# Optimization experiments

Hardware: AMD Instinct MI355X
Metric: run time of the kernel (lower is better)

The kernel has to match this reference:

```python
import jax, jax.numpy as jnp
import numpy as np
from jax import lax

TEMP = 0.1  # softmax_temp default in forward


def _conv(x, w, b):
    y = lax.conv_general_dilated(x, w, (1, 1), 'VALID',
                                 dimension_numbers=('NCHW', 'OIHW', 'NCHW'))
    return y + b[None, :, None, None]


def _avg_pool2(x):
    # AvgPool2d(2,2), floor mode (VALID window)
    s = lax.reduce_window(x, 0.0, lax.add, (1, 1, 2, 2), (1, 1, 2, 2), 'VALID')
    return s / 4.0


def _cnn(x, c1w, c1b, c2w, c2b, c3w, c3b, dw, db):
    x = _avg_pool2(jax.nn.relu(_conv(x, c1w, c1b)))   # (N,8,13,13)
    x = _avg_pool2(jax.nn.relu(_conv(x, c2w, c2b)))   # (N,16,5,5)
    x = _avg_pool2(jax.nn.relu(_conv(x, c3w, c3b)))   # (N,32,1,1)
    x = x.reshape(x.shape[0], -1)                      # (N,32)
    logits = x @ dw.T + db                             # (N,10)
    return jax.nn.softmax(logits, axis=1)


def _digit_to_rule(p):
    # p: (N,10) -> (N,6)
    return jnp.stack([p[:, 8], p[:, 4] + p[:, 6], p[:, 0] + p[:, 2],
                      p[:, 7] + p[:, 9], p[:, 5], p[:, 1] + p[:, 3]], axis=1)


def setup_inputs() -> dict:
    key = jax.random.key(0)
    ks = jax.random.split(key, 10)
    B, T, D, C, H, W = 256, 8, 4, 1, 28, 28
    sc = 0.1
    return {
        'sequences': jax.random.normal(ks[0], (B, T, D, C, H, W), jnp.float32),
        'conv1_w': jax.random.normal(ks[1], (8, 1, 3, 3), jnp.float32) * sc,
        'conv1_b': jax.random.normal(ks[2], (8,), jnp.float32) * sc,
        'conv2_w': jax.random.normal(ks[3], (16, 8, 3, 3), jnp.float32) * sc,
        'conv2_b': jax.random.normal(ks[4], (16,), jnp.float32) * sc,
        'conv3_w': jax.random.normal(ks[5], (32, 16, 3, 3), jnp.float32) * sc,
        'conv3_b': jax.random.normal(ks[6], (32,), jnp.float32) * sc,
        'dense_w': jax.random.normal(ks[7], (10, 32), jnp.float32) * sc,
        'dense_b': jax.random.normal(ks[8], (10,), jnp.float32) * sc,
        'trans': jax.nn.softmax(jax.random.normal(ks[9], (6, 9, 10), jnp.float32), axis=-1),
    }


def reference(sequences, conv1_w, conv1_b, conv2_w, conv2_b, conv3_w, conv3_b,
              dense_w, dense_b, trans):
    B, T, D, C, H, W = sequences.shape
    S = trans.shape[2]           # num_states = 10
    N = T * D                    # number of recurrence steps
    # CNN is independent per (t,d,b): batch all images at once.
    imgs = jnp.transpose(sequences, (1, 2, 0, 3, 4, 5)).reshape(N * B, C, H, W)
    digit_probs = _cnn(imgs, conv1_w, conv1_b, conv2_w, conv2_b,
                       conv3_w, conv3_b, dense_w, dense_b)      # (N*B,10)
    guard_probs = _digit_to_rule(digit_probs)                   # (N*B,6)

    # Per-rule transition matrices: softmax with temperature + fixed accepting row.
    M = jax.nn.softmax(trans / TEMP, axis=-1)                   # (R,S-1,S)
    acc = jnp.zeros((S,), M.dtype).at[-1].set(1.0)
    M = jnp.concatenate([M, jnp.broadcast_to(acc, (M.shape[0], 1, S))], axis=1)  # (R,S,S)

    # Effective transition matrices per step and batch element.
    g = guard_probs.reshape(N, B, -1)
    A_all = jnp.einsum('nbr,rij->nbij', g, M)                   # (N,B,S,S)

    state0 = jnp.zeros((B, S), sequences.dtype).at[:, 0].set(1.0)

    def step(state, A):
        return jnp.einsum('bi,bij->bj', state, A), None

    state_final, _ = lax.scan(step, state0, A_all)
    all_cnn_preds = digit_probs.reshape(N, B, -1)
    all_guard_preds = g
    return all_cnn_preds, all_guard_preds, state_final
```

## Files before the change

### kernel.cpp

```cpp
#include <hip/hip_runtime.h>

__global__ __launch_bounds__(256) void prep_kernel(
    const float* __restrict__ w2g, const float* __restrict__ w3g,
    const float* __restrict__ wdg, float* __restrict__ wsW)
{
    const int tid = threadIdx.x;
    for (int i = tid; i < 1152; i += 256) {
        int l = i & 3, c = (i >> 2) & 15, g = (i >> 6) & 1, k = i >> 7;
        wsW[i] = w2g[(c * 8 + g * 4 + l) * 9 + k];
    }
    for (int i = tid; i < 4608; i += 256) {
        int l = i & 3, c = (i >> 2) & 31, g = (i >> 7) & 3, k = i >> 9;
        wsW[1152 + i] = w3g[(c * 16 + g * 4 + l) * 9 + k];
    }
    for (int i = tid; i < 320; i += 256) {
        int j = i >> 5, c2 = i & 31;
        wsW[5760 + c2 * 10 + j] = wdg[i];
    }
}

__global__ __launch_bounds__(256) void cnn_kernel(
    const float* __restrict__ seq,
    const float* __restrict__ w1g, const float* __restrict__ b1g,
    const float* __restrict__ b2g, const float* __restrict__ b3g,
    const float* __restrict__ bdg, const float* __restrict__ wsW,
    float* __restrict__ out, float* __restrict__ g_ws)
{
    __shared__ __align__(16) float s_img2[4][28][28];
    __shared__ __align__(16) float s_p1n[4][2][10][11][4];
    __shared__ __align__(16) float s_p2n[4][16][16];
    __shared__ float s_c3[4][32][4];
    __shared__ float s_p3[4][32];
    __shared__ float s_logit[4][10];
    __shared__ float s_prob[4][10];

    const int tid   = threadIdx.x;
    const int mbase = blockIdx.x * 4;

    if (tid < 196) {
        #pragma unroll
        for (int img = 0; img < 4; img++) {
            const int m = mbase + img;
            const int b = m & 255, nn = m >> 8;
            const int t = nn >> 2, dd = nn & 3;
            const float4* s4 = (const float4*)(seq + (((size_t)b * 8 + t) * 4 + dd) * 784);
            float4 v = s4[tid];
            int flat = tid * 4;
            int r  = flat / 28;
            int cb = flat - r * 28;
            int e  = cb >> 1;
            *(float2*)&s_img2[img][r][e]      = make_float2(v.x, v.z);
            *(float2*)&s_img2[img][r][14 + e] = make_float2(v.y, v.w);
        }
    }
    __syncthreads();

    for (int idx = tid; idx < 400; idx += 256) {
        const int img = idx / 100;
        const int rem = idx - img * 100;
        const int y   = rem / 10;
        const int x   = rem - y * 10;
        const int r0  = 2 * y;
        float p[4][4];
        #pragma unroll
        for (int i = 0; i < 4; i++) {
            const float* rp = &s_img2[img][r0 + i][0];
            p[i][0] = rp[x];
            p[i][1] = rp[14 + x];
            p[i][2] = rp[x + 1];
            p[i][3] = rp[15 + x];
        }
        float res[8];
        #pragma unroll
        for (int c = 0; c < 8; c++) {
            float w[9];
            #pragma unroll
            for (int k = 0; k < 9; k++) w[k] = w1g[c * 9 + k];
            const float bias = b1g[c];
            float acc = 0.f;
            #pragma unroll
            for (int rr = 0; rr < 2; rr++)
                #pragma unroll
                for (int cc = 0; cc < 2; cc++) {
                    float v = bias;
                    #pragma unroll
                    for (int i = 0; i < 3; i++)
                        #pragma unroll
                        for (int j = 0; j < 3; j++)
                            v += p[rr + i][cc + j] * w[i * 3 + j];
                    acc += fmaxf(v, 0.f);
                }
            res[c] = 0.25f * acc;
        }
        const int slot = (x >> 1) + 5 * (x & 1);
        *(float4*)&s_p1n[img][0][y][slot][0] = make_float4(res[0], res[1], res[2], res[3]);
        *(float4*)&s_p1n[img][1][y][slot][0] = make_float4(res[4], res[5], res[6], res[7]);
    }
    __syncthreads();

    const int img2 = tid >> 6;
    const int t6   = tid & 63;

    {
        const int pos = t6 >> 2;
        const int q   = t6 & 3;
        const int y   = pos >> 2, x = pos & 3;
        const int r0  = 2 * y;
        const int slotm[4] = { x, 5 + x, x + 1, 6 + x };
        float v[4][4];
        #pragma unroll
        for (int oc = 0; oc < 4; oc++) {
            const float bias = b2g[q * 4 + oc];
            #pragma unroll
            for (int w2 = 0; w2 < 4; w2++) v[oc][w2] = bias;
        }
        #pragma unroll
        for (int g = 0; g < 2; g++) {
            float4 a[4][4];
            #pragma unroll
            for (int i = 0; i < 4; i++)
                #pragma unroll
                for (int dx = 0; dx < 4; dx++)
                    a[i][dx] = *(const float4*)&s_p1n[img2][g][r0 + i][slotm[dx]][0];
            #pragma unroll
            for (int k = 0; k < 9; k++) {
                const int di = k / 3, dj = k - di * 3;
                #pragma unroll
                for (int oc = 0; oc < 4; oc++) {
                    float4 wk = *(const float4*)&wsW[((k * 2 + g) * 16 + q * 4 + oc) * 4];
                    #pragma unroll
                    for (int rr = 0; rr < 2; rr++)
                        #pragma unroll
                        for (int cc = 0; cc < 2; cc++) {
                            float4 aa = a[rr + di][cc + dj];
                            v[oc][rr * 2 + cc] += aa.x * wk.x + aa.y * wk.y +
                                                  aa.z * wk.z + aa.w * wk.w;
                        }
                }
            }
        }
        float res[4];
        #pragma unroll
        for (int oc = 0; oc < 4; oc++)
            res[oc] = 0.25f * (fmaxf(v[oc][0], 0.f) + fmaxf(v[oc][1], 0.f) +
                               fmaxf(v[oc][2], 0.f) + fmaxf(v[oc][3], 0.f));
        *(float4*)&s_p2n[img2][pos][q * 4] = make_float4(res[0], res[1], res[2], res[3]);
    }
    __syncthreads();

    {
        const int c = t6 >> 1;
        const int u = t6 & 1;
        const float* w3n = wsW + 1152;
        float acc0 = b3g[c], acc1 = acc0;
        #pragma unroll
        for (int g = 0; g < 4; g++) {
            float4 A[3][4];
            #pragma unroll
            for (int i = 0; i < 3; i++)
                #pragma unroll
                for (int jj = 0; jj < 4; jj++)
                    A[i][jj] = *(const float4*)&s_p2n[img2][(u + i) * 4 + jj][g * 4];
            #pragma unroll
            for (int i = 0; i < 3; i++)
                #pragma unroll
                for (int j = 0; j < 3; j++) {
                    const int k = i * 3 + j;
                    float4 wk = *(const float4*)&w3n[((k * 4 + g) * 32 + c) * 4];
                    float4 a0 = A[i][j], a1 = A[i][j + 1];
                    acc0 += a0.x * wk.x + a0.y * wk.y + a0.z * wk.z + a0.w * wk.w;
                    acc1 += a1.x * wk.x + a1.y * wk.y + a1.z * wk.z + a1.w * wk.w;
                }
        }
        s_c3[img2][c][u * 2 + 0] = fmaxf(acc0, 0.f);
        s_c3[img2][c][u * 2 + 1] = fmaxf(acc1, 0.f);
    }
    __syncthreads();
    if (t6 < 32)
        s_p3[img2][t6] = 0.25f * (s_c3[img2][t6][0] + s_c3[img2][t6][1] +
                                  s_c3[img2][t6][2] + s_c3[img2][t6][3]);
    __syncthreads();

    if (t6 < 10) {
        const float* wdt = wsW + 5760;
        float acc = bdg[t6];
        #pragma unroll
        for (int c2 = 0; c2 < 32; c2++) acc += s_p3[img2][c2] * wdt[c2 * 10 + t6];
        s_logit[img2][t6] = acc;
    }
    __syncthreads();
    if (t6 < 10) {
        const int m = mbase + img2;
        float mx = s_logit[img2][0];
        #pragma unroll
        for (int k = 1; k < 10; k++) mx = fmaxf(mx, s_logit[img2][k]);
        float ssum = 0.f;
        #pragma unroll
        for (int k = 0; k < 10; k++) ssum += __expf(s_logit[img2][k] - mx);
        float p = __expf(s_logit[img2][t6] - mx) / ssum;
        s_prob[img2][t6] = p;
        out[(size_t)m * 10 + t6] = p;
    }
    __syncthreads();
    if (t6 < 6) {
        const int m = mbase + img2;
        int ia = (0x157048 >> (t6 * 4)) & 0xF;
        int ib = (0x3F926F >> (t6 * 4)) & 0xF;
        float gv = s_prob[img2][ia] + (ib < 10 ? s_prob[img2][ib] : 0.f);
        out[81920 + (size_t)m * 6 + t6] = gv;
        g_ws[(size_t)m * 6 + t6] = gv;
    }
}

__global__ __launch_bounds__(256) void sfa_kernel(
    const float* __restrict__ trans,
    const float* __restrict__ g_ws,
    float* __restrict__ out)
{
    __shared__ float M[600];
    const int tid  = threadIdx.x;
    const int lane = tid & 63;
    const int wv   = tid >> 6;

    if (tid < 54) {
        int r = tid / 9, i = tid - r * 9;
        const float* row = trans + (size_t)(r * 9 + i) * 10;
        float x[10], mx = -1e30f;
        #pragma unroll
        for (int j = 0; j < 10; j++) { x[j] = 10.f * row[j]; mx = fmaxf(mx, x[j]); }
        float s = 0.f;
        #pragma unroll
        for (int j = 0; j < 10; j++) { x[j] = __expf(x[j] - mx); s += x[j]; }
        float inv = 1.f / s;
        #pragma unroll
        for (int j = 0; j < 10; j++) M[(r * 9 + i) * 10 + j] = x[j] * inv;
    }
    __syncthreads();

    const int bb    = lane / 10;
    const int j     = lane - bb * 10;
    const int base  = bb * 10;
    const bool ok   = (bb < 6);
    int batch = blockIdx.x * 24 + wv * 6 + bb;
    const bool live = ok && (batch < 256);
    if (!live) batch = 0;

    float Mreg[54];
    #pragma unroll
    for (int k = 0; k < 54; k++) Mreg[k] = M[k * 10 + j];

    float stj = (j == 0) ? 1.f : 0.f;

    for (int nn = 0; nn < 32; nn++) {
        const float* gp = g_ws + ((size_t)nn * 256 + batch) * 6;
        float2 ga = *(const float2*)(gp);
        float2 gb = *(const float2*)(gp + 2);
        float2 gc = *(const float2*)(gp + 4);
        float g[6] = {ga.x, ga.y, gb.x, gb.y, gc.x, gc.y};

        float st[10];
        #pragma unroll
        for (int i = 0; i < 10; i++) st[i] = __shfl(stj, base + i, 64);

        float gsum = g[0] + g[1] + g[2] + g[3] + g[4] + g[5];
        float ns = (j == 9) ? gsum * st[9] : 0.f;
        #pragma unroll
        for (int r = 0; r < 6; r++) {
            float h = 0.f;
            #pragma unroll
            for (int i = 0; i < 9; i++) h += st[i] * Mreg[r * 9 + i];
            ns += g[r] * h;
        }
        stj = ns;
    }
    if (live) out[131072 + (size_t)batch * 10 + j] = stj;
}

extern "C" void kernel_launch(void* const* d_in, const int* in_sizes, int n_in,
                              void* d_out, int out_size, void* d_ws, size_t ws_size,
                              hipStream_t stream) {
    const float* seq = (const float*)d_in[0];
    const float* w1  = (const float*)d_in[1];
    const float* b1  = (const float*)d_in[2];
    const float* w2  = (const float*)d_in[3];
    const float* b2  = (const float*)d_in[4];
    const float* w3  = (const float*)d_in[5];
    const float* b3  = (const float*)d_in[6];
    const float* wd  = (const float*)d_in[7];
    const float* bd  = (const float*)d_in[8];
    const float* tr  = (const float*)d_in[9];
    float* out  = (float*)d_out;
    float* g_ws = (float*)d_ws;
    float* wsW  = g_ws + 49152;

    prep_kernel<<<1, 256, 0, stream>>>(w2, w3, wd, wsW);
    cnn_kernel<<<2048, 256, 0, stream>>>(seq, w1, b1, b2, b3, bd, wsW, out, g_ws);
    sfa_kernel<<<11, 256, 0, stream>>>(tr, g_ws, out);
}
```

Measured before the change: 156.2 us.

## Store CNN activations and conv2/conv3 weights in fp16, use fdot2

Converts the staged input image, the pooled conv1 and conv2 activations and the conv2/conv3 weights to fp16. The conv2 and conv3 inner products now use packed fdot2 with fp32 accumulation. The workspace is reshuffled so the dense weights stay fp32 at the front and the half-precision weights follow. This roughly halves LDS footprint and LDS/weight load traffic and halves the instruction count of the dot products. The cost is reduced precision on inputs and intermediates, which may push the output probabilities outside tolerance.

```diff
diff --git a/kernel.cpp b/kernel.cpp
--- a/kernel.cpp
+++ b/kernel.cpp
@@ -1,21 +1,35 @@
 #include <hip/hip_runtime.h>
+
+typedef _Float16 half_t;
+typedef _Float16 h2 __attribute__((ext_vector_type(2)));
+typedef _Float16 h4 __attribute__((ext_vector_type(4)));
+
+__device__ __forceinline__ float fdot2f(h2 a, h2 b, float c) {
+#if __has_builtin(__builtin_amdgcn_fdot2)
+    return __builtin_amdgcn_fdot2(a, b, c, false);
+#else
+    return c + (float)a.x * (float)b.x + (float)a.y * (float)b.y;
+#endif
+}
 
 __global__ __launch_bounds__(256) void prep_kernel(
     const float* __restrict__ w2g, const float* __restrict__ w3g,
     const float* __restrict__ wdg, float* __restrict__ wsW)
 {
     const int tid = threadIdx.x;
+    half_t* w2h = (half_t*)(wsW + 320);
+    half_t* w3h = w2h + 1152;
+    for (int i = tid; i < 320; i += 256) {
+        int j = i >> 5, c2 = i & 31;
+        wsW[c2 * 10 + j] = wdg[i];
+    }
     for (int i = tid; i < 1152; i += 256) {
         int l = i & 3, c = (i >> 2) & 15, g = (i >> 6) & 1, k = i >> 7;
-        wsW[i] = w2g[(c * 8 + g * 4 + l) * 9 + k];
+        w2h[i] = (half_t)w2g[(c * 8 + g * 4 + l) * 9 + k];
     }
     for (int i = tid; i < 4608; i += 256) {
         int l = i & 3, c = (i >> 2) & 31, g = (i >> 7) & 3, k = i >> 9;
-        wsW[1152 + i] = w3g[(c * 16 + g * 4 + l) * 9 + k];
-    }
-    for (int i = tid; i < 320; i += 256) {
-        int j = i >> 5, c2 = i & 31;
-        wsW[5760 + c2 * 10 + j] = wdg[i];
+        w3h[i] = (half_t)w3g[(c * 16 + g * 4 + l) * 9 + k];
     }
 }
 
@@ -26,9 +40,9 @@
     const float* __restrict__ bdg, const float* __restrict__ wsW,
     float* __restrict__ out, float* __restrict__ g_ws)
 {
-    __shared__ __align__(16) float s_img2[4][28][28];
-    __shared__ __align__(16) float s_p1n[4][2][10][11][4];
-    __shared__ __align__(16) float s_p2n[4][16][16];
+    __shared__ __align__(16) half_t s_img2[4][28][28];
+    __shared__ __align__(16) half_t s_p1n[4][2][10][11][4];
+    __shared__ __align__(16) half_t s_p2n[4][16][16];
     __shared__ float s_c3[4][32][4];
     __shared__ float s_p3[4][32];
     __shared__ float s_logit[4][10];
@@ -36,6 +50,9 @@
 
     const int tid   = threadIdx.x;
     const int mbase = blockIdx.x * 4;
+    const float*  wdt = wsW;
+    const half_t* w2h = (const half_t*)(wsW + 320);
+    const half_t* w3h = w2h + 1152;
 
     if (tid < 196) {
         #pragma unroll
@@ -49,8 +66,10 @@
             int r  = flat / 28;
             int cb = flat - r * 28;
             int e  = cb >> 1;
-            *(float2*)&s_img2[img][r][e]      = make_float2(v.x, v.z);
-            *(float2*)&s_img2[img][r][14 + e] = make_float2(v.y, v.w);
+            h2 ev = { (half_t)v.x, (half_t)v.z };
+            h2 od = { (half_t)v.y, (half_t)v.w };
+            *(h2*)&s_img2[img][r][e]      = ev;
+            *(h2*)&s_img2[img][r][14 + e] = od;
         }
     }
     __syncthreads();
@@ -64,11 +83,11 @@
         float p[4][4];
         #pragma unroll
         for (int i = 0; i < 4; i++) {
-            const float* rp = &s_img2[img][r0 + i][0];
-            p[i][0] = rp[x];
-            p[i][1] = rp[14 + x];
-            p[i][2] = rp[x + 1];
-            p[i][3] = rp[15 + x];
+            const half_t* rp = &s_img2[img][r0 + i][0];
+            p[i][0] = (float)rp[x];
+            p[i][1] = (float)rp[14 + x];
+            p[i][2] = (float)rp[x + 1];
+            p[i][3] = (float)rp[15 + x];
         }
         float res[8];
         #pragma unroll
@@ -93,8 +112,10 @@
             res[c] = 0.25f * acc;
         }
         const int slot = (x >> 1) + 5 * (x & 1);
-        *(float4*)&s_p1n[img][0][y][slot][0] = make_float4(res[0], res[1], res[2], res[3]);
-        *(float4*)&s_p1n[img][1][y][slot][0] = make_float4(res[4], res[5], res[6], res[7]);
+        h4 lo = { (half_t)res[0], (half_t)res[1], (half_t)res[2], (half_t)res[3] };
+        h4 hi = { (half_t)res[4], (half_t)res[5], (half_t)res[6], (half_t)res[7] };
+        *(h4*)&s_p1n[img][0][y][slot][0] = lo;
+        *(h4*)&s_p1n[img][1][y][slot][0] = hi;
     }
     __syncthreads();
 
@@ -116,25 +137,30 @@
         }
         #pragma unroll
         for (int g = 0; g < 2; g++) {
-            float4 a[4][4];
+            h2 aL[4][4], aH[4][4];
             #pragma unroll
             for (int i = 0; i < 4; i++)
                 #pragma unroll
-                for (int dx = 0; dx < 4; dx++)
-                    a[i][dx] = *(const float4*)&s_p1n[img2][g][r0 + i][slotm[dx]][0];
+                for (int dx = 0; dx < 4; dx++) {
+                    h4 a = *(const h4*)&s_p1n[img2][g][r0 + i][slotm[dx]][0];
+                    aL[i][dx] = __builtin_shufflevector(a, a, 0, 1);
+                    aH[i][dx] = __builtin_shufflevector(a, a, 2, 3);
+                }
             #pragma unroll
             for (int k = 0; k < 9; k++) {
                 const int di = k / 3, dj = k - di * 3;
                 #pragma unroll
                 for (int oc = 0; oc < 4; oc++) {
-                    float4 wk = *(const float4*)&wsW[((k * 2 + g) * 16 + q * 4 + oc) * 4];
+                    h4 w = *(const h4*)&w2h[((k * 2 + g) * 16 + q * 4 + oc) * 4];
+                    h2 wL = __builtin_shufflevector(w, w, 0, 1);
+                    h2 wH = __builtin_shufflevector(w, w, 2, 3);
                     #pragma unroll
                     for (int rr = 0; rr < 2; rr++)
                         #pragma unroll
                         for (int cc = 0; cc < 2; cc++) {
-                            float4 aa = a[rr + di][cc + dj];
-                            v[oc][rr * 2 + cc] += aa.x * wk.x + aa.y * wk.y +
-                                                  aa.z * wk.z + aa.w * wk.w;
+                            float* acc = &v[oc][rr * 2 + cc];
+                            *acc = fdot2f(aL[rr + di][cc + dj], wL, *acc);
+                            *acc = fdot2f(aH[rr + di][cc + dj], wH, *acc);
                         }
                 }
             }
@@ -144,32 +170,38 @@
         for (int oc = 0; oc < 4; oc++)
             res[oc] = 0.25f * (fmaxf(v[oc][0], 0.f) + fmaxf(v[oc][1], 0.f) +
                                fmaxf(v[oc][2], 0.f) + fmaxf(v[oc][3], 0.f));
-        *(float4*)&s_p2n[img2][pos][q * 4] = make_float4(res[0], res[1], res[2], res[3]);
+        h4 o = { (half_t)res[0], (half_t)res[1], (half_t)res[2], (half_t)res[3] };
+        *(h4*)&s_p2n[img2][pos][q * 4] = o;
     }
     __syncthreads();
 
     {
         const int c = t6 >> 1;
         const int u = t6 & 1;
-        const float* w3n = wsW + 1152;
         float acc0 = b3g[c], acc1 = acc0;
         #pragma unroll
         for (int g = 0; g < 4; g++) {
-            float4 A[3][4];
+            h2 AL[3][4], AH[3][4];
             #pragma unroll
             for (int i = 0; i < 3; i++)
                 #pragma unroll
-                for (int jj = 0; jj < 4; jj++)
-                    A[i][jj] = *(const float4*)&s_p2n[img2][(u + i) * 4 + jj][g * 4];
+                for (int jj = 0; jj < 4; jj++) {
+                    h4 a = *(const h4*)&s_p2n[img2][(u + i) * 4 + jj][g * 4];
+                    AL[i][jj] = __builtin_shufflevector(a, a, 0, 1);
+                    AH[i][jj] = __builtin_shufflevector(a, a, 2, 3);
+                }
             #pragma unroll
             for (int i = 0; i < 3; i++)
                 #pragma unroll
                 for (int j = 0; j < 3; j++) {
                     const int k = i * 3 + j;
-                    float4 wk = *(const float4*)&w3n[((k * 4 + g) * 32 + c) * 4];
-                    float4 a0 = A[i][j], a1 = A[i][j + 1];
-                    acc0 += a0.x * wk.x + a0.y * wk.y + a0.z * wk.z + a0.w * wk.w;
-                    acc1 += a1.x * wk.x + a1.y * wk.y + a1.z * wk.z + a1.w * wk.w;
+                    h4 w = *(const h4*)&w3h[((k * 4 + g) * 32 + c) * 4];
+                    h2 wL = __builtin_shufflevector(w, w, 0, 1);
+                    h2 wH = __builtin_shufflevector(w, w, 2, 3);
+                    acc0 = fdot2f(AL[i][j], wL, acc0);
+                    acc0 = fdot2f(AH[i][j], wH, acc0);
+                    acc1 = fdot2f(AL[i][j + 1], wL, acc1);
+                    acc1 = fdot2f(AH[i][j + 1], wH, acc1);
                 }
         }
         s_c3[img2][c][u * 2 + 0] = fmaxf(acc0, 0.f);
@@ -182,7 +214,6 @@
     __syncthreads();
 
     if (t6 < 10) {
-        const float* wdt = wsW + 5760;
         float acc = bdg[t6];
         #pragma unroll
         for (int c2 = 0; c2 < 32; c2++) acc += s_p3[img2][c2] * wdt[c2 * 10 + t6];
```

Result: faster. 148.7 us (-4.8%).
